# Optimization experiments

Measured on AMD Instinct MI355X. Metric: run time of the kernel, lower is better.

Reference implementation:

```python
import jax, jax.numpy as jnp
import numpy as np

T, B, E, H = 2048, 2, 1024, 16
D = E // H

def setup_inputs() -> dict:
    key = jax.random.key(0)
    ks = jax.random.split(key, 5)
    s = 1.0 / np.sqrt(E)  # keep projection weights at sane scale
    return {
        "query": jax.random.normal(ks[0], (T, B, E), jnp.float32),
        "Wq": jax.random.normal(ks[1], (E, E), jnp.float32) * s,
        "bq": jnp.zeros((E,), jnp.float32),
        "Wk": jax.random.normal(ks[2], (E, E), jnp.float32) * s,
        "bk": jnp.zeros((E,), jnp.float32),
        "Wv": jax.random.normal(ks[3], (E, E), jnp.float32) * s,
        "bv": jnp.zeros((E,), jnp.float32),
        "Wo": jax.random.normal(ks[4], (E, E), jnp.float32) * s,
        "bo": jnp.zeros((E,), jnp.float32),
    }

def reference(query, Wq, bq, Wk, bk, Wv, bv, Wo, bo):
    # query: [T, B, E] (fairseq time-first). self-attention path.
    scaling = D ** -0.5
    q = (query @ Wq.T + bq) * scaling          # [T,B,E]
    k = query @ Wk.T + bk                      # [T,B,E]
    v = query @ Wv.T + bv                      # [T,B,E]
    # split heads: [T,B,H,D]
    q = q.reshape(T, B, H, D)
    k = k.reshape(T, B, H, D)
    v = v.reshape(T, B, H, D)
    # attention scores [B,H,T,S]
    scores = jnp.einsum("tbhd,sbhd->bhts", q, k)
    probs = jax.nn.softmax(scores, axis=-1)
    # weighted values -> [T,B,H,D]
    attn = jnp.einsum("bhts,sbhd->tbhd", probs, v).reshape(T, B, E)
    return attn @ Wo.T + bo                    # [T,B,E]
```

## Files before the change

kernel.cpp:

```cpp
#include <hip/hip_runtime.h>
#include <hip/hip_bf16.h>

#define T_DIM 2048

typedef __attribute__((ext_vector_type(8))) short short8_t;
typedef short8_t __attribute__((may_alias)) short8_a;
typedef __attribute__((ext_vector_type(4))) short short4_t;
typedef short4_t __attribute__((may_alias)) short4_a;
typedef __attribute__((ext_vector_type(4))) float f32x4;
typedef __attribute__((ext_vector_type(16))) float f32x16;
typedef __attribute__((ext_vector_type(4))) float float4_t;
typedef float4_t __attribute__((may_alias)) float4_a;
typedef __attribute__((ext_vector_type(4))) unsigned int u32x4;

__device__ __forceinline__ short f2bf(float f) {
    unsigned int u = __builtin_bit_cast(unsigned int, f);
    unsigned int r = (u + 0x7fffu + ((u >> 16) & 1u)) >> 16;
    return (short)r;
}

__device__ __forceinline__ void gl_lds16(const short* g, short* l) {
    __builtin_amdgcn_global_load_lds(
        (const __attribute__((address_space(1))) void*)g,
        (__attribute__((address_space(3))) void*)l, 16, 0, 0);
}

__global__ __launch_bounds__(256) void cvt_all(const float* __restrict__ query,
                                               const float* __restrict__ Wq,
                                               const float* __restrict__ Wk,
                                               const float* __restrict__ Wv,
                                               const float* __restrict__ Wo,
                                               short* __restrict__ out) {
    const int bx = blockIdx.x;
    const int i = bx * 2048 + threadIdx.x * 8;
    const float* s;
    if (bx < 2048) {
        s = query + i;
    } else {
        int j = i - 4194304;
        int wsel = j >> 20;
        const float* wp = wsel == 0 ? Wq : (wsel == 1 ? Wk : (wsel == 2 ? Wv : Wo));
        s = wp + (j & 1048575);
    }
    float4_a a = *(const float4_a*)s;
    float4_a b = *(const float4_a*)(s + 4);
    short8_a r;
    r[0] = f2bf(a[0]); r[1] = f2bf(a[1]); r[2] = f2bf(a[2]); r[3] = f2bf(a[3]);
    r[4] = f2bf(b[0]); r[5] = f2bf(b[1]); r[6] = f2bf(b[2]); r[7] = f2bf(b[3]);
    *(short8_a*)(out + i) = r;
}

template <int BM, int BN, int MODE>
__global__ __launch_bounds__(256) void gemm_lds(const short* __restrict__ A,
                                                const short* __restrict__ W,
                                                const float* __restrict__ b0,
                                                const float* __restrict__ b1,
                                                const float* __restrict__ b2,
                                                short* __restrict__ o0,
                                                short* __restrict__ o1,
                                                short* __restrict__ o2,
                                                float* __restrict__ of) {
    constexpr int FM = BM / 32;
    constexpr int FN = BN / 32;
    __shared__ short As[BM * 32];
    __shared__ short Bs[BN * 32];

    const int tid = threadIdx.x;
    const int l = tid & 63, w = tid >> 6;
    const int wm = w >> 1, wn = w & 1;

    const int nbx = gridDim.x;
    const int nb = nbx * gridDim.y;
    const int bid = blockIdx.x + nbx * blockIdx.y;
    const int swz = (bid & 7) * (nb >> 3) + (bid >> 3);
    const int bx = swz % nbx, by = swz / nbx;

    const int m0 = by * BM, n0 = bx * BN;
    const int l15 = l & 15, l4 = l >> 4;
    const int lr = l >> 2, lc = (l & 3) * 8;

    f32x4 acc[FM][FN];
#pragma unroll
    for (int i = 0; i < FM; i++)
#pragma unroll
        for (int j = 0; j < FN; j++) {
            f32x4 z = {0.f, 0.f, 0.f, 0.f};
            acc[i][j] = z;
        }

    const short* Ab = A + (m0 + lr) * 1024 + lc;
    const short* Wb = W + (n0 + lr) * 1024 + lc;

    for (int k0 = 0; k0 < 1024; k0 += 32) {
#pragma unroll
        for (int j = 0; j < BM / 64; j++) {
            int base = (j * 4 + w) * 16;
            gl_lds16(Ab + base * 1024 + k0, &As[base * 32]);
        }
#pragma unroll
        for (int j = 0; j < BN / 64; j++) {
            int base = (j * 4 + w) * 16;
            gl_lds16(Wb + base * 1024 + k0, &Bs[base * 32]);
        }
        __syncthreads();

        short8_t af[FM], bf[FN];
#pragma unroll
        for (int m = 0; m < FM; m++)
            af[m] = *(const short8_a*)&As[(wm * (BM / 2) + m * 16 + l15) * 32 + l4 * 8];
#pragma unroll
        for (int n = 0; n < FN; n++)
            bf[n] = *(const short8_a*)&Bs[(wn * (BN / 2) + n * 16 + l15) * 32 + l4 * 8];
#pragma unroll
        for (int m = 0; m < FM; m++)
#pragma unroll
            for (int n = 0; n < FN; n++)
                acc[m][n] = __builtin_amdgcn_mfma_f32_16x16x32_bf16(af[m], bf[n], acc[m][n], 0, 0, 0);
        __syncthreads();
    }

    if (MODE == 3) {
#pragma unroll
        for (int n = 0; n < FN; n++) {
            int col = n0 + wn * (BN / 2) + n * 16 + l15;
            float bv = b0[col];
#pragma unroll
            for (int m = 0; m < FM; m++)
#pragma unroll
                for (int i = 0; i < 4; i++) {
                    int row = m0 + wm * (BM / 2) + m * 16 + l4 * 4 + i;
                    of[row * 1024 + col] = acc[m][n][i] + bv;
                }
        }
    } else {
        const int proj = n0 >> 10;
        const float* bias = proj == 0 ? b0 : (proj == 1 ? b1 : b2);
        short* outp = proj == 0 ? o0 : (proj == 1 ? o1 : o2);
#pragma unroll
        for (int n = 0; n < FN; n++) {
            int cw = (n0 + wn * (BN / 2) + n * 16 + l15) & 1023;
            float bv = bias[cw];
            int h = cw >> 6, d = cw & 63;
#pragma unroll
            for (int m = 0; m < FM; m++)
#pragma unroll
                for (int i = 0; i < 4; i++) {
                    int row = m0 + wm * (BM / 2) + m * 16 + l4 * 4 + i;
                    float v = acc[m][n][i] + bv;
                    if (proj == 0) v *= 0.18033688011112042f;
                    int bb = row & 1, t = row >> 1;
                    int bh = bb * 16 + h;
                    if (proj == 0)
                        outp[(bh * 2048 + t) * 64 + d] = f2bf(v);
                    else if (proj == 1)
                        outp[bh * 131072 + (t >> 6) * 4096 + (d >> 3) * 512 + (t & 63) * 8 + (d & 7)] = f2bf(v);
                    else
                        outp[bh * 131072 + (t >> 6) * 4096 + ((t & 63) >> 3) * 512 + d * 8 + (t & 7)] = f2bf(v);
                }
        }
    }
}

__global__ __launch_bounds__(512, 4) void flash_attn(const short* __restrict__ Q,
                                                     const short* __restrict__ K,
                                                     const short* __restrict__ Vt,
                                                     short* __restrict__ O) {
    __shared__ short Ks[4][64 * 64];
    __shared__ short Vs[6][64 * 64];

    const int tid = threadIdx.x, l = tid & 63, w = tid >> 6;
    const int w4 = w >> 1, g = w & 1;
    const int l31 = l & 31, hi = l >> 5;

    const int bid = blockIdx.x + (blockIdx.y << 4);
    const int swz = (bid & 7) * 64 + (bid >> 3);
    const int qt = swz & 15, bh = swz >> 4;

    const int b = bh >> 4, hh = bh & 15;
    const int qrow = qt * 128 + w4 * 32 + l31;

    const short* Qp = Q + bh * (T_DIM * 64);
    const short* Kp = K + bh * 131072;
    const short* Vp = Vt + bh * 131072;

    short8_t qf[4];
#pragma unroll
    for (int c = 0; c < 4; c++)
        qf[c] = *(const short8_a*)&Qp[qrow * 64 + c * 16 + hi * 8];

    f32x16 oacc[2];
    f32x16 lacc;
#pragma unroll
    for (int i = 0; i < 16; i++) { oacc[0][i] = 0.f; oacc[1][i] = 0.f; lacc[i] = 0.f; }

    short8_t ones;
#pragma unroll
    for (int j = 0; j < 8; j++) ones[j] = (short)0x3F80;

    const int wq = w & 3;
    const int p0 = 2 * wq, p1 = 2 * wq + 1;
    const short* sgK0 = Kp + p0 * 512 + l * 8;
    const short* sgK1 = Kp + p1 * 512 + l * 8;
    const short* sgV0 = Vp + p0 * 512 + l * 8;
    const short* sgV1 = Vp + p1 * 512 + l * 8;

    auto stage = [&](int t) {
        const int off = t * 4096;
        if (w < 4) {
            const int buf = t & 3;
            gl_lds16(sgK0 + off, &Ks[buf][p0 * 512]);
            gl_lds16(sgK1 + off, &Ks[buf][p1 * 512]);
        } else {
            const int buf = t % 6;
            gl_lds16(sgV0 + off, &Vs[buf][p0 * 512]);
            gl_lds16(sgV1 + off, &Vs[buf][p1 * 512]);
        }
    };

    auto qkhalf = [&](f32x16& s, int t, int r) {
        const short* kc = &Ks[t & 3][0];
#pragma unroll
        for (int c = 0; c < 4; c++) {
            short8_t kf = *(const short8_a*)&kc[(2 * c + hi) * 512 + (r * 32 + l31) * 8];
            if (c == 0) {
                f32x16 z;
#pragma unroll
                for (int i = 0; i < 16; i++) z[i] = 0.f;
                s = __builtin_amdgcn_mfma_f32_32x32x16_bf16(kf, qf[0], z, 0, 0, 0);
            } else {
                s = __builtin_amdgcn_mfma_f32_32x32x16_bf16(kf, qf[c], s, 0, 0, 0);
            }
        }
    };

    auto expackhalf = [&](f32x16& s, short8_t* pf2) {
#pragma unroll
        for (int i = 0; i < 16; i++) s[i] = exp2f(s[i]);
        unsigned pk8[8];
#pragma unroll
        for (int u = 0; u < 8; u++) {
            unsigned t;
            asm("v_cvt_pk_bf16_f32 %0, %1, %2" : "=v"(t) : "v"(s[2 * u]), "v"(s[2 * u + 1]));
            pk8[u] = t;
        }
#pragma unroll
        for (int cc = 0; cc < 2; cc++) {
            unsigned A0 = pk8[4 * cc + 0], B0 = pk8[4 * cc + 2];
            unsigned A1 = pk8[4 * cc + 1], B1 = pk8[4 * cc + 3];
            asm("v_permlane32_swap_b32 %0, %1" : "+v"(A0), "+v"(B0));
            asm("v_permlane32_swap_b32 %0, %1" : "+v"(A1), "+v"(B1));
            u32x4 pu = {A0, A1, B0, B1};
            pf2[cc] = __builtin_bit_cast(short8_t, pu);
        }
    };

    auto pv = [&](const short8_t* pf, int t) {
        const short* vc = &Vs[t % 6][0];
#pragma unroll
        for (int r = 0; r < 2; r++)
#pragma unroll
            for (int cc = 0; cc < 2; cc++) {
                short8_t p = pf[r * 2 + cc];
                lacc = __builtin_amdgcn_mfma_f32_32x32x16_bf16(ones, p, lacc, 0, 0, 0);
#pragma unroll
                for (int dd = 0; dd < 2; dd++) {
                    short8_t vf = *(const short8_a*)&vc[(4 * r + 2 * cc + hi) * 512 +
                                                        (dd * 32 + l31) * 8];
                    oacc[dd] = __builtin_amdgcn_mfma_f32_32x32x16_bf16(vf, p, oacc[dd], 0, 0, 0);
                }
            }
    };

    stage(0);
    stage(1);

    short8_t pfA[4], pfB[4];

    auto body = [&](int p, short8_t* pfIn, short8_t* pfOut) {
        __syncthreads();
        if (p < 15) { stage(2 * p + 2); stage(2 * p + 3); }
        const int t = 2 * p + g;
        f32x16 sa, sb;
        __builtin_amdgcn_s_setprio(1);
        qkhalf(sa, t, 0);
        qkhalf(sb, t, 1);
        if (p > 0) pv(pfIn, t - 2);
        __builtin_amdgcn_s_setprio(0);
        expackhalf(sa, &pfOut[0]);
        expackhalf(sb, &pfOut[2]);
    };

    for (int p = 0; p < 16; p += 2) {
        body(p, pfB, pfA);
        body(p + 1, pfA, pfB);
    }
    pv(pfB, 30 + g);

    __syncthreads();
    float* xo = (float*)&Ks[0][0];
    float* xml = (float*)&Vs[0][0];
    if (g == 1) {
#pragma unroll
        for (int dd = 0; dd < 2; dd++)
#pragma unroll
            for (int g4 = 0; g4 < 4; g4++) {
                f32x4 v = {oacc[dd][4 * g4], oacc[dd][4 * g4 + 1],
                           oacc[dd][4 * g4 + 2], oacc[dd][4 * g4 + 3]};
                *(float4_a*)&xo[w4 * 2048 + (dd * 4 + g4) * 256 + l * 4] = v;
            }
        xml[w4 * 64 + l] = lacc[0];
    }
    __syncthreads();
    if (g == 0) {
        float rl = 1.0f / (lacc[0] + xml[w4 * 64 + l]);
#pragma unroll
        for (int dd = 0; dd < 2; dd++)
#pragma unroll
            for (int g4 = 0; g4 < 4; g4++) {
                f32x4 o1 = *(const float4_a*)&xo[w4 * 2048 + (dd * 4 + g4) * 256 + l * 4];
                short4_t o4;
#pragma unroll
                for (int i = 0; i < 4; i++)
                    o4[i] = f2bf((oacc[dd][4 * g4 + i] + o1[i]) * rl);
                *(short4_a*)&O[(qrow * 2 + b) * 1024 + hh * 64 + dd * 32 + g4 * 8 + hi * 4] = o4;
            }
    }
}

extern "C" void kernel_launch(void* const* d_in, const int* in_sizes, int n_in,
                              void* d_out, int out_size, void* d_ws, size_t ws_size,
                              hipStream_t stream) {
    const float* query = (const float*)d_in[0];
    const float* Wq = (const float*)d_in[1];
    const float* bq = (const float*)d_in[2];
    const float* Wk = (const float*)d_in[3];
    const float* bk = (const float*)d_in[4];
    const float* Wv = (const float*)d_in[5];
    const float* bv = (const float*)d_in[6];
    const float* Wo = (const float*)d_in[7];
    const float* bo = (const float*)d_in[8];

    short* Xbf = (short*)d_ws;
    short* Wqb = Xbf + 4194304;
    short* Wkb = Wqb + 1048576;
    short* Wvb = Wkb + 1048576;
    short* Wob = Wvb + 1048576;
    short* Qb = Wob + 1048576;
    short* Kb = Qb + 4194304;
    short* Vtb = Kb + 4194304;
    short* attnb = Xbf;

    cvt_all<<<4096, 256, 0, stream>>>(query, Wq, Wk, Wv, Wo, Xbf);

    gemm_lds<128, 128, 4><<<dim3(24, 32), 256, 0, stream>>>(Xbf, Wqb, bq, bk, bv,
                                                            Qb, Kb, Vtb, nullptr);

    flash_attn<<<dim3(16, 32), 512, 0, stream>>>(Qb, Kb, Vtb, attnb);

    gemm_lds<64, 128, 3><<<dim3(8, 64), 256, 0, stream>>>(attnb, Wob, bo, nullptr, nullptr,
                                                          nullptr, nullptr, nullptr, (float*)d_out);
}
```

Measured before the change: 137.5 us.

## Replace ones-MFMA row-sum with VALU accumulation and interleave QK/exp halves

Drops the extra MFMA that multiplied P by a ones matrix to get softmax row sums. The sums are now accumulated in fp32 on the VALU inside the exp loop and combined across lane halves with a shuffle at the end. The attention body is reordered so the exp/pack of the first QK half runs before the PV MFMAs and the second QK half, using one score accumulator instead of two. This trades matrix-core work and registers for extra VALU adds and a different overlap pattern. The row sum is now taken from fp32 values rather than the rounded bf16 P, which changes numerics slightly.

```diff
diff --git a/kernel.cpp b/kernel.cpp
--- a/kernel.cpp
+++ b/kernel.cpp
@@ -189,13 +189,9 @@
         qf[c] = *(const short8_a*)&Qp[qrow * 64 + c * 16 + hi * 8];
 
     f32x16 oacc[2];
-    f32x16 lacc;
-#pragma unroll
-    for (int i = 0; i < 16; i++) { oacc[0][i] = 0.f; oacc[1][i] = 0.f; lacc[i] = 0.f; }
-
-    short8_t ones;
-#pragma unroll
-    for (int j = 0; j < 8; j++) ones[j] = (short)0x3F80;
+#pragma unroll
+    for (int i = 0; i < 16; i++) { oacc[0][i] = 0.f; oacc[1][i] = 0.f; }
+    float rsum = 0.f;
 
     const int wq = w & 3;
     const int p0 = 2 * wq, p1 = 2 * wq + 1;
@@ -234,8 +230,15 @@
     };
 
     auto expackhalf = [&](f32x16& s, short8_t* pf2) {
-#pragma unroll
-        for (int i = 0; i < 16; i++) s[i] = exp2f(s[i]);
+        float r0 = 0.f, r1 = 0.f, r2 = 0.f, r3 = 0.f;
+#pragma unroll
+        for (int i = 0; i < 4; i++) {
+            s[4 * i] = exp2f(s[4 * i]);         r0 += s[4 * i];
+            s[4 * i + 1] = exp2f(s[4 * i + 1]); r1 += s[4 * i + 1];
+            s[4 * i + 2] = exp2f(s[4 * i + 2]); r2 += s[4 * i + 2];
+            s[4 * i + 3] = exp2f(s[4 * i + 3]); r3 += s[4 * i + 3];
+        }
+        rsum += (r0 + r1) + (r2 + r3);
         unsigned pk8[8];
 #pragma unroll
         for (int u = 0; u < 8; u++) {
@@ -261,7 +264,6 @@
 #pragma unroll
             for (int cc = 0; cc < 2; cc++) {
                 short8_t p = pf[r * 2 + cc];
-                lacc = __builtin_amdgcn_mfma_f32_32x32x16_bf16(ones, p, lacc, 0, 0, 0);
 #pragma unroll
                 for (int dd = 0; dd < 2; dd++) {
                     short8_t vf = *(const short8_a*)&vc[(4 * r + 2 * cc + hi) * 512 +
@@ -280,14 +282,16 @@
         __syncthreads();
         if (p < 15) { stage(2 * p + 2); stage(2 * p + 3); }
         const int t = 2 * p + g;
-        f32x16 sa, sb;
+        f32x16 s;
         __builtin_amdgcn_s_setprio(1);
-        qkhalf(sa, t, 0);
-        qkhalf(sb, t, 1);
+        qkhalf(s, t, 0);
+        __builtin_amdgcn_s_setprio(0);
+        expackhalf(s, &pfOut[0]);
+        __builtin_amdgcn_s_setprio(1);
         if (p > 0) pv(pfIn, t - 2);
+        qkhalf(s, t, 1);
         __builtin_amdgcn_s_setprio(0);
-        expackhalf(sa, &pfOut[0]);
-        expackhalf(sb, &pfOut[2]);
+        expackhalf(s, &pfOut[2]);
     };
 
     for (int p = 0; p < 16; p += 2) {
@@ -295,6 +299,8 @@
         body(p + 1, pfA, pfB);
     }
     pv(pfB, 30 + g);
+
+    float lsum = rsum + __shfl_xor(rsum, 32);
 
     __syncthreads();
     float* xo = (float*)&Ks[0][0];
@@ -308,11 +314,11 @@
                            oacc[dd][4 * g4 + 2], oacc[dd][4 * g4 + 3]};
                 *(float4_a*)&xo[w4 * 2048 + (dd * 4 + g4) * 256 + l * 4] = v;
             }
-        xml[w4 * 64 + l] = lacc[0];
+        xml[w4 * 64 + l] = lsum;
     }
     __syncthreads();
     if (g == 0) {
-        float rl = 1.0f / (lacc[0] + xml[w4 * 64 + l]);
+        float rl = 1.0f / (lsum + xml[w4 * 64 + l]);
 #pragma unroll
         for (int dd = 0; dd < 2; dd++)
 #pragma unroll
```

After: 154.6 us. +12.5%, slower.
